# Kernel optimization log

Hardware: AMD Instinct MI355X
Metric: run time of the kernel (lower is better)

## Reference

```python
import jax, jax.numpy as jnp
import numpy as np

N = 50000
IN_CH = 128
OUT_CH = 64
HEADS = 4
NEG_SLOPE = 0.2


def _gatv2(x, src, dst, W_l, W_r, att):
    """GATv2Conv, concat=False, no bias/residual/dropout.
    x: [N, in]; src/dst: [E]; W_l/W_r: [in, H*C]; att: [H, C].
    Returns [N, C] (mean over heads)."""
    n = x.shape[0]
    xl = (x @ W_l).reshape(n, HEADS, OUT_CH)
    xr = (x @ W_r).reshape(n, HEADS, OUT_CH)
    # per-edge message: x_j (source, lin_l) + x_i (target, lin_r)
    m = jax.nn.leaky_relu(xl[src] + xr[dst], negative_slope=NEG_SLOPE)  # [E,H,C]
    e = jnp.einsum('ehc,hc->eh', m, att)  # [E,H]
    # segment softmax over incoming edges of each dst node
    emax = jax.ops.segment_max(e, dst, num_segments=n)  # [N,H] (-inf for empty)
    ex = jnp.exp(e - emax[dst])
    denom = jax.ops.segment_sum(ex, dst, num_segments=n)  # [N,H]
    alpha = ex / denom[dst]
    out = jax.ops.segment_sum(alpha[:, :, None] * xl[src], dst, num_segments=n)  # [N,H,C]
    return out.mean(axis=1)


def setup_inputs() -> dict:
    key = jax.random.key(0)
    ks = jax.random.split(key, 9)
    E = 800000
    s = 1.0 / np.sqrt(IN_CH)
    return {
        'x': jax.random.normal(ks[0], (N, IN_CH), dtype=jnp.float32),
        'edge_index1': jax.random.randint(ks[1], (2, E), 0, N, dtype=jnp.int64),
        'edge_index2': jax.random.randint(ks[2], (2, E), 0, N, dtype=jnp.int64),
        'W_l': jax.random.normal(ks[3], (IN_CH, HEADS * OUT_CH), dtype=jnp.float32) * s,  # shared lin_l
        'W_r0': jax.random.normal(ks[4], (IN_CH, HEADS * OUT_CH), dtype=jnp.float32) * s,
        'W_r1': jax.random.normal(ks[5], (IN_CH, HEADS * OUT_CH), dtype=jnp.float32) * s,
        'att0': jax.random.normal(ks[6], (HEADS, OUT_CH), dtype=jnp.float32) * (1.0 / np.sqrt(OUT_CH)),
        'att1': jax.random.normal(ks[7], (HEADS, OUT_CH), dtype=jnp.float32) * (1.0 / np.sqrt(OUT_CH)),
        'theta': jnp.zeros((1,), dtype=jnp.float32),
    }


def reference(x, edge_index1, edge_index2, W_l, W_r0, W_r1, att0, att1, theta):
    n = x.shape[0]
    # hop 0: add self loops
    loop = jnp.arange(n, dtype=edge_index1.dtype)
    src0 = jnp.concatenate([edge_index1[0], loop])
    dst0 = jnp.concatenate([edge_index1[1], loop])
    out = _gatv2(x, src0, dst0, W_l, W_r0, att0)
    # hop 1: no self loops, gated residual sum
    out = out + jax.nn.sigmoid(theta[0]) * _gatv2(x, edge_index2[0], edge_index2[1], W_l, W_r1, att1)
    return out
```

## Files before the change

kernel.cpp:

```cpp
#include <hip/hip_runtime.h>
#include <hip/hip_bf16.h>
#include <math.h>

#define IN_CH   128
#define HC      256
#define OUT_C   64

typedef unsigned short ushort_t;
typedef __attribute__((ext_vector_type(2))) float v2f;
typedef __attribute__((ext_vector_type(4))) float v4f;
typedef __attribute__((ext_vector_type(8))) short bf16x8;

__device__ __forceinline__ ushort_t f2bf_rne(float f) {
    unsigned u = __float_as_uint(f);
    unsigned r = (u + 0x7FFFu + ((u >> 16) & 1u)) >> 16;
    return (ushort_t)r;
}
__device__ __forceinline__ v2f bfpair(unsigned u) {
    v2f r;
    r.x = __uint_as_float(u << 16);
    r.y = __uint_as_float(u & 0xffff0000u);
    return r;
}
__device__ __forceinline__ v2f vmax0(v2f a) {
    v2f r;
    r.x = fmaxf(a.x, 0.f);
    r.y = fmaxf(a.y, 0.f);
    return r;
}

__device__ __forceinline__ float4 ntld4(const float* p) {
    v4f t = __builtin_nontemporal_load((const v4f*)p);
    return make_float4(t.x, t.y, t.z, t.w);
}
__device__ __forceinline__ int ntldi(const int* p) {
    return __builtin_nontemporal_load(p);
}
__device__ __forceinline__ void ntst4(float* p, float4 v) {
    v4f t = {v.x, v.y, v.z, v.w};
    __builtin_nontemporal_store(t, (v4f*)p);
}
__device__ __forceinline__ void ntsti(int* p, int v) {
    __builtin_nontemporal_store(v, p);
}

#define DPP_ROR_ADD(x, N)                                                   \
    (x) += __uint_as_float(__builtin_amdgcn_update_dpp(                     \
        0, __float_as_uint(x), 0x120 + (N), 0xF, 0xF, true))

__device__ __forceinline__ float rowsum16(float x) {
    DPP_ROR_ADD(x, 8);
    DPP_ROR_ADD(x, 4);
    DPP_ROR_ADD(x, 2);
    DPP_ROR_ADD(x, 1);
    return x;
}

__device__ __forceinline__ bf16x8 ldbf(const uint4* p) {
    union { uint4 u; bf16x8 v; } t;
    t.u = *p;
    return t.v;
}

__device__ __forceinline__ void dev_gemm(const float* __restrict__ x,
                                         const float* __restrict__ W,
                                         float* __restrict__ outf,
                                         ushort_t* __restrict__ outh,
                                         int n, int bx) {
    const int tid = threadIdx.x;
    const int c4  = tid & 63;
    const int rg  = __builtin_amdgcn_readfirstlane(tid >> 6);
    const int row0 = bx * 64 + rg * 16;
    const int nm1 = n - 1;
    const float4* Wv = (const float4*)W;
    const float* xr[16];
#pragma unroll
    for (int j = 0; j < 16; ++j) {
        int r = row0 + j;
        xr[j] = x + (size_t)(r > nm1 ? nm1 : r) * IN_CH;
    }
    v2f acc[16][2];
#pragma unroll
    for (int j = 0; j < 16; ++j) {
        acc[j][0] = (v2f){0.f, 0.f};
        acc[j][1] = (v2f){0.f, 0.f};
    }
    for (int k = 0; k < IN_CH; k += 4) {
        const float4 w0 = Wv[(k + 0) * 64 + c4];
        const float4 w1 = Wv[(k + 1) * 64 + c4];
        const float4 w2 = Wv[(k + 2) * 64 + c4];
        const float4 w3 = Wv[(k + 3) * 64 + c4];
        const v2f w0a = {w0.x, w0.y}, w0b = {w0.z, w0.w};
        const v2f w1a = {w1.x, w1.y}, w1b = {w1.z, w1.w};
        const v2f w2a = {w2.x, w2.y}, w2b = {w2.z, w2.w};
        const v2f w3a = {w3.x, w3.y}, w3b = {w3.z, w3.w};
#pragma unroll
        for (int jb = 0; jb < 2; ++jb) {
            float4 xv[8];
#pragma unroll
            for (int j = 0; j < 8; ++j) xv[j] = *(const float4*)(xr[jb * 8 + j] + k);
#pragma unroll
            for (int j = 0; j < 8; ++j) {
                const int a = jb * 8 + j;
                const v2f s0 = {xv[j].x, xv[j].x}, s1 = {xv[j].y, xv[j].y};
                const v2f s2 = {xv[j].z, xv[j].z}, s3 = {xv[j].w, xv[j].w};
                acc[a][0] = s0 * w0a + acc[a][0];
                acc[a][1] = s0 * w0b + acc[a][1];
                acc[a][0] = s1 * w1a + acc[a][0];
                acc[a][1] = s1 * w1b + acc[a][1];
                acc[a][0] = s2 * w2a + acc[a][0];
                acc[a][1] = s2 * w2b + acc[a][1];
                acc[a][0] = s3 * w3a + acc[a][0];
                acc[a][1] = s3 * w3b + acc[a][1];
            }
        }
    }
#pragma unroll
    for (int j = 0; j < 16; ++j) {
        const int row = row0 + j;
        if (row < n) {
            if (outh) {
                ushort4 h;
                h.x = f2bf_rne(acc[j][0].x);
                h.y = f2bf_rne(acc[j][0].y);
                h.z = f2bf_rne(acc[j][1].x);
                h.w = f2bf_rne(acc[j][1].y);
                ((ushort4*)(outh + (size_t)row * HC))[c4] = h;
            } else {
                ntst4(outf + (size_t)row * HC + 4 * c4,
                      make_float4(acc[j][0].x, acc[j][0].y, acc[j][1].x, acc[j][1].y));
            }
        }
    }
}

__device__ __forceinline__ void dev_scatter_rank(const int* __restrict__ src1,
                                                 const int* __restrict__ dst1, int E1,
                                                 const int* __restrict__ src2,
                                                 const int* __restrict__ dst2, int E2,
                                                 int n, const int* __restrict__ offs,
                                                 const int* __restrict__ rank,
                                                 int* __restrict__ csr,
                                                 int bid, int nB) {
    const int Et = E1 + E2;
    for (int i = bid * 256 + threadIdx.x; i < Et; i += nB * 256) {
        if (i < E1) {
            csr[offs[ntldi(dst1 + i)] + ntldi(rank + i)] = ntldi(src1 + i) << 9;
        } else {
            int j = i - E1;
            csr[offs[n + ntldi(dst2 + j)] + ntldi(rank + i)] = ntldi(src2 + j) << 9;
        }
    }
}

__global__ __launch_bounds__(256) void k_prep(const float* __restrict__ x,
                                              const float* __restrict__ Wl,
                                              const float* __restrict__ Wr0,
                                              const float* __restrict__ Wr1,
                                              uint4* __restrict__ xAh,
                                              uint4* __restrict__ xAl,
                                              uint4* __restrict__ WBh,
                                              uint4* __restrict__ WBl,
                                              int n, int GH, int gPX,
                                              const int* __restrict__ dst1, int E1,
                                              const int* __restrict__ dst2, int E2,
                                              int* __restrict__ deg,
                                              int* __restrict__ rank) {
    const int bx = blockIdx.x;
    if (bx < GH) {
        const int Et = E1 + E2;
        for (int i = bx * 256 + threadIdx.x; i < Et; i += GH * 256) {
            if (i < E1) ntsti(rank + i, atomicAdd(&deg[ntldi(dst1 + i)], 1));
            else        ntsti(rank + i, atomicAdd(&deg[n + ntldi(dst2 + i - E1)], 1));
        }
        return;
    }
    const int t = bx - GH;
    float v[8];
    ushort_t h[8], l[8];
    if (t < gPX) {
        const int idx = t * 256 + threadIdx.x;
        const int row = idx >> 4;
        const int ko  = idx & 15;
        float4 v0 = make_float4(0.f, 0.f, 0.f, 0.f), v1 = v0;
        if (row < n) {
            const float4* xp = (const float4*)(x + (size_t)row * IN_CH + ko * 8);
            v0 = xp[0];
            v1 = xp[1];
        }
        v[0] = v0.x; v[1] = v0.y; v[2] = v0.z; v[3] = v0.w;
        v[4] = v1.x; v[5] = v1.y; v[6] = v1.z; v[7] = v1.w;
#pragma unroll
        for (int j = 0; j < 8; ++j) {
            h[j] = f2bf_rne(v[j]);
            l[j] = f2bf_rne(v[j] - __uint_as_float((unsigned)h[j] << 16));
        }
        const int di = ((row >> 4) * 4 + (ko >> 2)) * 64 + ((ko & 3) << 4) + (row & 15);
        uint4 ph, pl;
        ph.x = (unsigned)h[0] | ((unsigned)h[1] << 16);
        ph.y = (unsigned)h[2] | ((unsigned)h[3] << 16);
        ph.z = (unsigned)h[4] | ((unsigned)h[5] << 16);
        ph.w = (unsigned)h[6] | ((unsigned)h[7] << 16);
        pl.x = (unsigned)l[0] | ((unsigned)l[1] << 16);
        pl.y = (unsigned)l[2] | ((unsigned)l[3] << 16);
        pl.z = (unsigned)l[4] | ((unsigned)l[5] << 16);
        pl.w = (unsigned)l[6] | ((unsigned)l[7] << 16);
        xAh[di] = ph;
        xAl[di] = pl;
    } else {
        const int idx = (t - gPX) * 256 + threadIdx.x;
        const int lane = idx & 63;
        const int f    = (idx >> 6) & 15;
        const int c    = (idx >> 10) & 3;
        const int w    = idx >> 12;
        if (w >= 3) return;
        const float* Wp = (w == 0) ? Wl : ((w == 1) ? Wr0 : Wr1);
        const int col = f * 16 + (lane & 15);
        const int k0  = c * 32 + (lane >> 4) * 8;
#pragma unroll
        for (int j = 0; j < 8; ++j) {
            v[j] = Wp[(size_t)(k0 + j) * HC + col];
            h[j] = f2bf_rne(v[j]);
            l[j] = f2bf_rne(v[j] - __uint_as_float((unsigned)h[j] << 16));
        }
        uint4 ph, pl;
        ph.x = (unsigned)h[0] | ((unsigned)h[1] << 16);
        ph.y = (unsigned)h[2] | ((unsigned)h[3] << 16);
        ph.z = (unsigned)h[4] | ((unsigned)h[5] << 16);
        ph.w = (unsigned)h[6] | ((unsigned)h[7] << 16);
        pl.x = (unsigned)l[0] | ((unsigned)l[1] << 16);
        pl.y = (unsigned)l[2] | ((unsigned)l[3] << 16);
        pl.z = (unsigned)l[4] | ((unsigned)l[5] << 16);
        pl.w = (unsigned)l[6] | ((unsigned)l[7] << 16);
        WBh[idx] = ph;
        WBl[idx] = pl;
    }
}

__global__ __launch_bounds__(256) void k_gemm3(const uint4* __restrict__ xAh,
                                               const uint4* __restrict__ xAl,
                                               const uint4* __restrict__ WBh,
                                               const uint4* __restrict__ WBl,
                                               ushort_t* __restrict__ xlh,
                                               float* __restrict__ xr0,
                                               float* __restrict__ xr1,
                                               int n, int GS,
                                               const int* __restrict__ src1,
                                               const int* __restrict__ dst1, int E1,
                                               const int* __restrict__ src2,
                                               const int* __restrict__ dst2, int E2,
                                               const int* __restrict__ offs,
                                               const int* __restrict__ rank,
                                               int* __restrict__ csr) {
    const int bx = blockIdx.x;
    if (bx < GS) {
        dev_scatter_rank(src1, dst1, E1, src2, dst2, E2, n, offs, rank, csr, bx, GS);
        return;
    }
    const int t    = bx - GS;
    const int tile = t / 3;
    const int wsel = t - tile * 3;

    const int lane = threadIdx.x & 63;
    const int wave = __builtin_amdgcn_readfirstlane((int)(threadIdx.x >> 6));

    v4f acc[4][4];
#pragma unroll
    for (int g = 0; g < 4; ++g)
#pragma unroll
        for (int f = 0; f < 4; ++f) acc[g][f] = (v4f){0.f, 0.f, 0.f, 0.f};

    const uint4* Bh = WBh + (size_t)wsel * 4096;
    const uint4* Bl = WBl + (size_t)wsel * 4096;
    const int g0 = tile * 4;

    for (int c = 0; c < 4; ++c) {
        bf16x8 ah[4], al[4], bh[4], bl[4];
#pragma unroll
        for (int g = 0; g < 4; ++g) {
            const int ai = ((g0 + g) * 4 + c) * 64 + lane;
            ah[g] = ldbf(xAh + ai);
            al[g] = ldbf(xAl + ai);
        }
#pragma unroll
        for (int f = 0; f < 4; ++f) {
            const int bi = (c * 16 + wave * 4 + f) * 64 + lane;
            bh[f] = ldbf(Bh + bi);
            bl[f] = ldbf(Bl + bi);
        }
#pragma unroll
        for (int g = 0; g < 4; ++g)
#pragma unroll
            for (int f = 0; f < 4; ++f) {
                acc[g][f] = __builtin_amdgcn_mfma_f32_16x16x32_bf16(ah[g], bh[f], acc[g][f], 0, 0, 0);
                acc[g][f] = __builtin_amdgcn_mfma_f32_16x16x32_bf16(ah[g], bl[f], acc[g][f], 0, 0, 0);
                acc[g][f] = __builtin_amdgcn_mfma_f32_16x16x32_bf16(al[g], bh[f], acc[g][f], 0, 0, 0);
            }
    }

    const int colB = wave * 64 + (lane & 15);
    const int rowB = tile * 64 + ((lane >> 4) << 2);
    if (wsel == 0) {
#pragma unroll
        for (int g = 0; g < 4; ++g)
#pragma unroll
            for (int f = 0; f < 4; ++f) {
                const int col = colB + f * 16;
#pragma unroll
                for (int r = 0; r < 4; ++r) {
                    const int row = rowB + g * 16 + r;
                    if (row < n) xlh[(size_t)row * HC + col] = f2bf_rne(acc[g][f][r]);
                }
            }
    } else {
        float* o = (wsel == 1) ? xr0 : xr1;
#pragma unroll
        for (int g = 0; g < 4; ++g)
#pragma unroll
            for (int f = 0; f < 4; ++f) {
                const int col = colB + f * 16;
#pragma unroll
                for (int r = 0; r < 4; ++r) {
                    const int row = rowB + g * 16 + r;
                    if (row < n)
                        __builtin_nontemporal_store(acc[g][f][r], o + (size_t)row * HC + col);
                }
            }
    }
}

__global__ __launch_bounds__(256) void k_aggboth(const ushort_t* __restrict__ xlh,
                                                 const float* __restrict__ xr0,
                                                 const float* __restrict__ xr1,
                                                 const float* __restrict__ att0,
                                                 const float* __restrict__ att1,
                                                 const int* __restrict__ offs,
                                                 const int* __restrict__ deg,
                                                 const int* __restrict__ csr,
                                                 int n, float* __restrict__ out,
                                                 const float* __restrict__ theta) {
    const int lane = threadIdx.x & 63;
    int node_ = blockIdx.x * 4 + (threadIdx.x >> 6);
    if (node_ >= n) return;
    const int node = __builtin_amdgcn_readfirstlane(node_);

    const float4 at0 = ((const float4*)att0)[lane];
    const float4 at1 = ((const float4*)att1)[lane];
    const v2f a2_0a = {0.2f * at0.x, 0.2f * at0.y}, a2_0b = {0.2f * at0.z, 0.2f * at0.w};
    const v2f a8_0a = {0.8f * at0.x, 0.8f * at0.y}, a8_0b = {0.8f * at0.z, 0.8f * at0.w};
    const v2f a2_1a = {0.2f * at1.x, 0.2f * at1.y}, a2_1b = {0.2f * at1.z, 0.2f * at1.w};
    const v2f a8_1a = {0.8f * at1.x, 0.8f * at1.y}, a8_1b = {0.8f * at1.z, 0.8f * at1.w};
    const float4 q0 = ntld4(xr0 + (size_t)node * HC + 4 * lane);
    const float4 q1 = ntld4(xr1 + (size_t)node * HC + 4 * lane);
    const v2f x0a = {q0.x, q0.y}, x0b = {q0.z, q0.w};
    const v2f x1a = {q1.x, q1.y}, x1b = {q1.z, q1.w};

    const int t0 = deg[node];
    const int s0 = offs[node];
    const int t1 = deg[n + node];
    const int s1 = offs[n + node];

    const char* Xc = (const char*)xlh;
    const unsigned laneB = (unsigned)lane * 8u;
    auto gat = [&](int off) -> uint2 {
        return *(const uint2*)(Xc + (unsigned)off + laneB);
    };

    float l0 = 0.f, l1 = 0.f;
    v2f O0a = {0.f, 0.f}, O0b = {0.f, 0.f};
    v2f O1a = {0.f, 0.f}, O1b = {0.f, 0.f};

    auto proc = [&](uint2 w, const v2f& xa, const v2f& xb,
                    const v2f& a8a, const v2f& a8b,
                    const v2f& a2a, const v2f& a2b, float& l, v2f& Oa, v2f& Ob) {
        v2f ca = bfpair(w.x), cb = bfpair(w.y);
        v2f za = ca + xa, zb = cb + xb;
        v2f t = a2a * za + a2b * zb + a8a * vmax0(za) + a8b * vmax0(zb);
        float part = rowsum16(t.x + t.y);
        float p = __expf(fminf(part, 60.f));
        l += p;
        v2f pp = {p, p};
        Oa = pp * ca + Oa;
        Ob = pp * cb + Ob;
    };
    auto proc0 = [&](uint2 w) { proc(w, x0a, x0b, a8_0a, a8_0b, a2_0a, a2_0b, l0, O0a, O0b); };
    auto proc1 = [&](uint2 w) { proc(w, x1a, x1b, a8_1a, a8_1b, a2_1a, a2_1b, l1, O1a, O1b); };

    proc0(gat(node << 9));

    auto ld0 = [&](int i) -> uint2 { return gat(ntldi(csr + s0 + i)); };
    auto ld1 = [&](int i) -> uint2 { return gat(ntldi(csr + s1 + i)); };

    uint2 a0 = ld0(0), a1 = ld0(1), a2 = ld0(2), a3 = ld0(3);
    uint2 b0 = ld1(0), b1 = ld1(1), b2 = ld1(2), b3 = ld1(3);

    const int k = t0 < t1 ? t0 : t1;
    int i = 0;
    for (; i + 2 <= k; i += 2) {
        uint2 c0 = a0, c1 = a1, d0 = b0, d1 = b1;
        a0 = a2; a1 = a3;
        b0 = b2; b1 = b3;
        a2 = ld0(i + 4);
        b2 = ld1(i + 4);
        a3 = ld0(i + 5);
        b3 = ld1(i + 5);
        proc0(c0);
        proc1(d0);
        proc0(c1);
        proc1(d1);
    }
    for (int i0 = i; i0 < t0; ++i0) {
        uint2 c = a0;
        a0 = a1; a1 = a2; a2 = a3;
        a3 = ld0(i0 + 4);
        proc0(c);
    }
    for (int i1 = i; i1 < t1; ++i1) {
        uint2 c = b0;
        b0 = b1; b1 = b2; b2 = b3;
        b3 = ld1(i1 + 4);
        proc1(c);
    }

    const float inv0 = 0.25f / l0;
    const float inv1 = (l1 > 0.f) ? 0.25f / l1 : 0.f;
    const float sg = 1.f / (1.f + __expf(-theta[0]));
    float vx = O0a.x * inv0 + sg * (O1a.x * inv1);
    float vy = O0a.y * inv0 + sg * (O1a.y * inv1);
    float vz = O0b.x * inv0 + sg * (O1b.x * inv1);
    float vw = O0b.y * inv0 + sg * (O1b.y * inv1);
    vx += __shfl_xor(vx, 16); vx += __shfl_xor(vx, 32);
    vy += __shfl_xor(vy, 16); vy += __shfl_xor(vy, 32);
    vz += __shfl_xor(vz, 16); vz += __shfl_xor(vz, 32);
    vw += __shfl_xor(vw, 16); vw += __shfl_xor(vw, 32);

    if (lane < 16) {
        ntst4(out + (size_t)node * OUT_C + 4 * lane, make_float4(vx, vy, vz, vw));
    }
}

__device__ __forceinline__ void dev_agg(const ushort_t* __restrict__ xlh,
                                        const float* __restrict__ xr,
                                        const float* __restrict__ att,
                                        const int* __restrict__ offs,
                                        const int* __restrict__ deg,
                                        const int* __restrict__ csr_src,
                                        int n, float* __restrict__ out,
                                        int selfLoop,
                                        const float* __restrict__ theta,
                                        int accumulate, int bid) {
    const int lane = threadIdx.x & 63;
    const int node = bid * 4 + (threadIdx.x >> 6);
    if (node >= n) return;

    const float4 attv = ((const float4*)att)[lane];
    const v2f a2a = {0.2f * attv.x, 0.2f * attv.y}, a2b = {0.2f * attv.z, 0.2f * attv.w};
    const v2f a8a = {0.8f * attv.x, 0.8f * attv.y}, a8b = {0.8f * attv.z, 0.8f * attv.w};
    const float4 q = ntld4(xr + (size_t)node * HC + 4 * lane);
    const v2f xa = {q.x, q.y}, xb = {q.z, q.w};
    const int start2 = offs[node] - selfLoop;
    const int total  = deg[node] + selfLoop;

    float l = 0.f;
    v2f Oa = {0.f, 0.f}, Ob = {0.f, 0.f};
    const char* Xc = (const char*)xlh;
    const unsigned laneB = (unsigned)lane * 8u;

    auto ld = [&](int i) -> uint2 {
        int off = (selfLoop && i == 0) ? (node << 9) : ntldi(csr_src + start2 + i);
        return *(const uint2*)(Xc + (unsigned)off + laneB);
    };
    auto process = [&](uint2 w) {
        v2f ca = bfpair(w.x), cb = bfpair(w.y);
        v2f za = ca + xa, zb = cb + xb;
        v2f t = a2a * za + a2b * zb + a8a * vmax0(za) + a8b * vmax0(zb);
        float part = rowsum16(t.x + t.y);
        float p = __expf(fminf(part, 60.f));
        l += p;
        v2f pp = {p, p};
        Oa = pp * ca + Oa;
        Ob = pp * cb + Ob;
    };

    if (total > 0) {
        uint2 b0 = ld(0);
        uint2 b1 = ld(1);
        uint2 b2 = ld(2);
        uint2 b3 = ld(3);
        int i = 0;
        for (; i + 4 <= total; i += 4) {
            uint2 c0 = b0, c1 = b1, c2 = b2, c3 = b3;
            b0 = ld(i + 4);
            b1 = ld(i + 5);
            b2 = ld(i + 6);
            b3 = ld(i + 7);
            process(c0);
            process(c1);
            process(c2);
            process(c3);
        }
        const int rem = total - i;
        if (rem > 0) process(b0);
        if (rem > 1) process(b1);
        if (rem > 2) process(b2);
    }

    float inv = (l > 0.f) ? 0.25f / l : 0.f;
    float vx = Oa.x * inv, vy = Oa.y * inv, vz = Ob.x * inv, vw = Ob.y * inv;
    vx += __shfl_xor(vx, 16); vx += __shfl_xor(vx, 32);
    vy += __shfl_xor(vy, 16); vy += __shfl_xor(vy, 32);
    vz += __shfl_xor(vz, 16); vz += __shfl_xor(vz, 32);
    vw += __shfl_xor(vw, 16); vw += __shfl_xor(vw, 32);

    if (lane < 16) {
        float4 r = make_float4(vx, vy, vz, vw);
        float4* op = (float4*)(out + (size_t)node * OUT_C);
        if (accumulate) {
            float sg = 1.f / (1.f + __expf(-theta[0]));
            float4 cur = op[lane];
            r.x = fmaf(sg, r.x, cur.x);
            r.y = fmaf(sg, r.y, cur.y);
            r.z = fmaf(sg, r.z, cur.z);
            r.w = fmaf(sg, r.w, cur.w);
        }
        op[lane] = r;
    }
}

__global__ __launch_bounds__(256) void k_mix1(const float* __restrict__ x,
                                              const float* __restrict__ Wa,
                                              ushort_t* __restrict__ oah,
                                              const float* __restrict__ Wb,
                                              float* __restrict__ ob, int n,
                                              int GH, int gG,
                                              const int* __restrict__ dst1, int E1,
                                              const int* __restrict__ dst2, int E2,
                                              int* __restrict__ deg,
                                              int* __restrict__ rank) {
    const int bx = blockIdx.x;
    if (bx < GH) {
        const int Et = E1 + E2;
        for (int i = bx * 256 + threadIdx.x; i < Et; i += GH * 256) {
            if (i < E1) ntsti(rank + i, atomicAdd(&deg[ntldi(dst1 + i)], 1));
            else        ntsti(rank + i, atomicAdd(&deg[n + ntldi(dst2 + i - E1)], 1));
        }
    } else {
        int t = bx - GH;
        if (t < gG) dev_gemm(x, Wa, nullptr, oah, n, t);
        else        dev_gemm(x, Wb, ob, nullptr, n, t - gG);
    }
}

__global__ __launch_bounds__(256) void k_mix2(const float* __restrict__ x,
                                              const float* __restrict__ Wc,
                                              float* __restrict__ oc, int n,
                                              int GS,
                                              const int* __restrict__ src1,
                                              const int* __restrict__ dst1, int E1,
                                              const int* __restrict__ src2,
                                              const int* __restrict__ dst2, int E2,
                                              const int* __restrict__ offs,
                                              const int* __restrict__ rank,
                                              int* __restrict__ csr) {
    const int bx = blockIdx.x;
    if (bx < GS)
        dev_scatter_rank(src1, dst1, E1, src2, dst2, E2, n, offs, rank, csr, bx, GS);
    else
        dev_gemm(x, Wc, oc, nullptr, n, bx - GS);
}

__global__ __launch_bounds__(256) void k_mix3(const ushort_t* __restrict__ xlh,
                                              const float* __restrict__ xr,
                                              const float* __restrict__ att,
                                              const int* __restrict__ offs,
                                              const int* __restrict__ deg,
                                              const int* __restrict__ csr_src,
                                              int n, float* __restrict__ out,
                                              int selfLoop,
                                              const float* __restrict__ theta,
                                              int accumulate) {
    dev_agg(xlh, xr, att, offs, deg, csr_src, n, out, selfLoop, theta,
            accumulate, blockIdx.x);
}

__global__ void k_zero(int* p, int n, int* q, int qn) {
    int i = blockIdx.x * 256 + threadIdx.x;
    if (i < n) p[i] = 0;
    if (blockIdx.x == 0 && threadIdx.x < (unsigned)qn) q[threadIdx.x] = 0;
}

__global__ __launch_bounds__(1024) void k_scanA(const int* __restrict__ deg, int n,
                                                int* __restrict__ incl,
                                                int* __restrict__ bsum) {
    __shared__ int sm[1024];
    const int t = threadIdx.x;
    const int i = blockIdx.x * 1024 + t;
    sm[t] = (i < n) ? deg[i] : 0;
    for (int off = 1; off < 1024; off <<= 1) {
        __syncthreads();
        int u = (t >= off) ? sm[t - off] : 0;
        __syncthreads();
        sm[t] += u;
    }
    if (i < n) incl[i] = sm[t];
    if (t == 1023) bsum[blockIdx.x] = sm[1023];
}

__global__ __launch_bounds__(1024) void k_scanB(int* __restrict__ bsum, int nb) {
    __shared__ int sm[1024];
    const int t = threadIdx.x;
    sm[t] = (t < nb) ? bsum[t] : 0;
    for (int off = 1; off < 1024; off <<= 1) {
        __syncthreads();
        int u = (t >= off) ? sm[t - off] : 0;
        __syncthreads();
        sm[t] += u;
    }
    if (t < nb) bsum[t] = sm[t];
}

__global__ void k_scanCf(const int* __restrict__ incl, const int* __restrict__ deg,
                         const int* __restrict__ bsum, int nb, int n,
                         int* __restrict__ offs) {
    __shared__ int sb[128];
    const int t = threadIdx.x;
    if (t < 128) sb[t] = (t < nb) ? bsum[t] : 0;
    __syncthreads();
#pragma unroll
    for (int off = 1; off < 128; off <<= 1) {
        int u = (t >= off && t < 128) ? sb[t - off] : 0;
        __syncthreads();
        if (t < 128) sb[t] += u;
        __syncthreads();
    }
    int i = blockIdx.x * 256 + t;
    if (i < n) {
        int b    = i >> 10;
        int base = (b > 0) ? sb[b - 1] : 0;
        offs[i] = base + incl[i] - deg[i];
    }
}

__global__ void k_scanC(const int* __restrict__ incl, const int* __restrict__ deg,
                        const int* __restrict__ bsum, int n,
                        int* __restrict__ offs) {
    int i = blockIdx.x * 256 + threadIdx.x;
    if (i < n) {
        int b    = i >> 10;
        int base = (b > 0) ? bsum[b - 1] : 0;
        offs[i] = base + incl[i] - deg[i];
    }
}

extern "C" void kernel_launch(void* const* d_in, const int* in_sizes, int n_in,
                              void* d_out, int out_size, void* d_ws, size_t ws_size,
                              hipStream_t stream) {
    const float* x     = (const float*)d_in[0];
    const int*   e1    = (const int*)d_in[1];
    const int*   e2    = (const int*)d_in[2];
    const float* Wl    = (const float*)d_in[3];
    const float* Wr0   = (const float*)d_in[4];
    const float* Wr1   = (const float*)d_in[5];
    const float* att0  = (const float*)d_in[6];
    const float* att1  = (const float*)d_in[7];
    const float* theta = (const float*)d_in[8];

    const int n  = in_sizes[0] / IN_CH;
    const int E1 = in_sizes[1] / 2;
    const int E2 = in_sizes[2] / 2;
    float* out = (float*)d_out;

    char* w = (char*)d_ws;
    auto alloc = [&](size_t bytes) -> char* {
        char* p = w;
        w += (bytes + 255) & ~(size_t)255;
        return p;
    };
    auto al = [](size_t b) -> size_t { return (b + 255) & ~(size_t)255; };

    const int gT = (n + 63) / 64;
    const size_t projH = (size_t)n * HC * 2;
    const size_t projF = (size_t)n * HC * 4;
    const size_t eB    = (size_t)(E1 + E2) * 4 + 64;
    const size_t degB  = (size_t)2 * n * 4;
    const size_t xAB   = (size_t)gT * 1024 * 16;
    const size_t WBB   = (size_t)3 * 4 * 16 * 64 * 16;

    const size_t need3 = al(projH) + 2 * al(projF) + 2 * al(eB) + 3 * al(degB) + 4096;
    const size_t needM = need3 + 2 * al(xAB) + 2 * al(WBB);
    const bool mfmaPath = ws_size >= needM;
    const bool threeBuf = ws_size >= need3;

    ushort_t* xlh = (ushort_t*)alloc(projH);
    float* xr0 = (float*)alloc(projF);
    float* xr1 = threeBuf ? (float*)alloc(projF) : xr0;
    int* csr  = (int*)alloc(eB);
    int* rank = (int*)alloc(eB);
    int* deg  = (int*)alloc(degB);
    int* offs = (int*)alloc(degB);
    int* tmp  = (int*)alloc(degB);
    int* bsum = (int*)alloc(4096);

    const int GA    = (n + 3) / 4;
    const int GH    = 2048;
    const int GS    = 2048;
    const int n2    = 2 * n;
    const int gN2   = (n2 + 255) / 256;
    const int nScan = (n2 + 1023) / 1024;

    if (mfmaPath) {
        uint4* xAh = (uint4*)alloc(xAB);
        uint4* xAl = (uint4*)alloc(xAB);
        uint4* WBh = (uint4*)alloc(WBB);
        uint4* WBl = (uint4*)alloc(WBB);
        const int gPX = gT * 4;
        const int gPW = 48;

        k_zero<<<gN2, 256, 0, stream>>>(deg, n2, csr + E1 + E2, 16);
        k_prep<<<GH + gPX + gPW, 256, 0, stream>>>(x, Wl, Wr0, Wr1,
                                                   xAh, xAl, WBh, WBl,
                                                   n, GH, gPX,
                                                   e1 + E1, E1, e2 + E2, E2,
                                                   deg, rank);
        k_scanA<<<nScan, 1024, 0, stream>>>(deg, n2, tmp, bsum);
        if (nScan <= 128) {
            k_scanCf<<<gN2, 256, 0, stream>>>(tmp, deg, bsum, nScan, n2, offs);
        } else {
            k_scanB<<<1, 1024, 0, stream>>>(bsum, nScan);
            k_scanC<<<gN2, 256, 0, stream>>>(tmp, deg, bsum, n2, offs);
        }
        k_gemm3<<<GS + 3 * gT, 256, 0, stream>>>(xAh, xAl, WBh, WBl,
                                                 xlh, xr0, xr1, n, GS,
                                                 e1, e1 + E1, E1, e2, e2 + E2, E2,
                                                 offs, rank, csr);
        k_aggboth<<<GA, 256, 0, stream>>>(xlh, xr0, xr1, att0, att1,
                                          offs, deg, csr, n, out, theta);
        return;
    }

    const int gG = gT;
    k_zero<<<gN2, 256, 0, stream>>>(deg, n2, csr + E1 + E2, 16);
    k_mix1<<<GH + 2 * gG, 256, 0, stream>>>(x, Wl, xlh, Wr0, xr0, n, GH, gG,
                                            e1 + E1, E1, e2 + E2, E2, deg, rank);
    k_scanA<<<nScan, 1024, 0, stream>>>(deg, n2, tmp, bsum);
    if (nScan <= 128) {
        k_scanCf<<<gN2, 256, 0, stream>>>(tmp, deg, bsum, nScan, n2, offs);
    } else {
        k_scanB<<<1, 1024, 0, stream>>>(bsum, nScan);
        k_scanC<<<gN2, 256, 0, stream>>>(tmp, deg, bsum, n2, offs);
    }

    if (threeBuf) {
        k_mix2<<<GS + gG, 256, 0, stream>>>(x, Wr1, xr1, n, GS,
                                            e1, e1 + E1, E1, e2, e2 + E2, E2,
                                            offs, rank, csr);
        k_aggboth<<<GA, 256, 0, stream>>>(xlh, xr0, xr1, att0, att1,
                                          offs, deg, csr, n, out, theta);
    } else {
        k_mix2<<<GS, 256, 0, stream>>>(x, Wr1, xr1, n, GS,
                                       e1, e1 + E1, E1, e2, e2 + E2, E2,
                                       offs, rank, csr);
        k_mix3<<<GA, 256, 0, stream>>>(xlh, xr0, att0, offs, deg, csr, n, out,
                                       1, theta, 0);
        k_mix2<<<gG, 256, 0, stream>>>(x, Wr1, xr0, n, 0,
                                       (const int*)nullptr, (const int*)nullptr, 0,
                                       (const int*)nullptr, (const int*)nullptr, 0,
                                       (const int*)nullptr, (const int*)nullptr,
                                       (int*)nullptr);
        k_mix3<<<GA, 256, 0, stream>>>(xlh, xr0, att1, offs + n, deg + n, csr, n, out,
                                       0, theta, 1);
    }
}
```

Measured before the change: 390.5 us.

## Batch CSR index loads per wavefront with readlane broadcast; split prep kernel

The aggregation loop now loads 64 CSR neighbour indices at once, one per lane, and broadcasts each with readlane. It then issues eight independent row gathers before processing them. This replaces the per-edge scalar index loads and the interleaved two-hop software pipeline, aiming for more memory-level parallelism and fewer dependent index loads. The fused prep kernel is split into separate pack and histogram kernels, and the CSR padding is enlarged to 64 entries so the 64-wide index reads stay in bounds. The two hops are now processed sequentially rather than interleaved, and the kernel split adds a launch.

```diff
diff --git a/kernel.cpp b/kernel.cpp
--- a/kernel.cpp
+++ b/kernel.cpp
@@ -153,7 +153,19 @@
     }
 }
 
-__global__ __launch_bounds__(256) void k_prep(const float* __restrict__ x,
+__global__ __launch_bounds__(256) void k_hist(int n, int GH,
+                                              const int* __restrict__ dst1, int E1,
+                                              const int* __restrict__ dst2, int E2,
+                                              int* __restrict__ deg,
+                                              int* __restrict__ rank) {
+    const int Et = E1 + E2;
+    for (int i = blockIdx.x * 256 + threadIdx.x; i < Et; i += GH * 256) {
+        if (i < E1) ntsti(rank + i, atomicAdd(&deg[ntldi(dst1 + i)], 1));
+        else        ntsti(rank + i, atomicAdd(&deg[n + ntldi(dst2 + i - E1)], 1));
+    }
+}
+
+__global__ __launch_bounds__(256) void k_pack(const float* __restrict__ x,
                                               const float* __restrict__ Wl,
                                               const float* __restrict__ Wr0,
                                               const float* __restrict__ Wr1,
@@ -161,21 +173,8 @@
                                               uint4* __restrict__ xAl,
                                               uint4* __restrict__ WBh,
                                               uint4* __restrict__ WBl,
-                                              int n, int GH, int gPX,
-                                              const int* __restrict__ dst1, int E1,
-                                              const int* __restrict__ dst2, int E2,
-                                              int* __restrict__ deg,
-                                              int* __restrict__ rank) {
-    const int bx = blockIdx.x;
-    if (bx < GH) {
-        const int Et = E1 + E2;
-        for (int i = bx * 256 + threadIdx.x; i < Et; i += GH * 256) {
-            if (i < E1) ntsti(rank + i, atomicAdd(&deg[ntldi(dst1 + i)], 1));
-            else        ntsti(rank + i, atomicAdd(&deg[n + ntldi(dst2 + i - E1)], 1));
-        }
-        return;
-    }
-    const int t = bx - GH;
+                                              int n, int gPX) {
+    const int t = blockIdx.x;
     float v[8];
     ushort_t h[8], l[8];
     if (t < gPX) {
@@ -362,8 +361,9 @@
 
     const char* Xc = (const char*)xlh;
     const unsigned laneB = (unsigned)lane * 8u;
-    auto gat = [&](int off) -> uint2 {
-        return *(const uint2*)(Xc + (unsigned)off + laneB);
+    auto gath = [&](unsigned off) -> uint2 {
+        const char* p = Xc + off;
+        return *(const uint2*)(p + laneB);
     };
 
     float l0 = 0.f, l1 = 0.f;
@@ -386,40 +386,54 @@
     auto proc0 = [&](uint2 w) { proc(w, x0a, x0b, a8_0a, a8_0b, a2_0a, a2_0b, l0, O0a, O0b); };
     auto proc1 = [&](uint2 w) { proc(w, x1a, x1b, a8_1a, a8_1b, a2_1a, a2_1b, l1, O1a, O1b); };
 
-    proc0(gat(node << 9));
-
-    auto ld0 = [&](int i) -> uint2 { return gat(ntldi(csr + s0 + i)); };
-    auto ld1 = [&](int i) -> uint2 { return gat(ntldi(csr + s1 + i)); };
-
-    uint2 a0 = ld0(0), a1 = ld0(1), a2 = ld0(2), a3 = ld0(3);
-    uint2 b0 = ld1(0), b1 = ld1(1), b2 = ld1(2), b3 = ld1(3);
-
-    const int k = t0 < t1 ? t0 : t1;
-    int i = 0;
-    for (; i + 2 <= k; i += 2) {
-        uint2 c0 = a0, c1 = a1, d0 = b0, d1 = b1;
-        a0 = a2; a1 = a3;
-        b0 = b2; b1 = b3;
-        a2 = ld0(i + 4);
-        b2 = ld1(i + 4);
-        a3 = ld0(i + 5);
-        b3 = ld1(i + 5);
-        proc0(c0);
-        proc1(d0);
-        proc0(c1);
-        proc1(d1);
-    }
-    for (int i0 = i; i0 < t0; ++i0) {
-        uint2 c = a0;
-        a0 = a1; a1 = a2; a2 = a3;
-        a3 = ld0(i0 + 4);
-        proc0(c);
-    }
-    for (int i1 = i; i1 < t1; ++i1) {
-        uint2 c = b0;
-        b0 = b1; b1 = b2; b2 = b3;
-        b3 = ld1(i1 + 4);
-        proc1(c);
+    proc0(gath((unsigned)node << 9));
+
+    for (int base = 0; base < t0; base += 64) {
+        const unsigned vc = (unsigned)csr[s0 + base + lane];
+        const int m = (t0 - base < 64) ? (t0 - base) : 64;
+        int j = 0;
+        for (; j + 8 <= m; j += 8) {
+            uint2 g0 = gath((unsigned)__builtin_amdgcn_readlane(vc, j + 0));
+            uint2 g1 = gath((unsigned)__builtin_amdgcn_readlane(vc, j + 1));
+            uint2 g2 = gath((unsigned)__builtin_amdgcn_readlane(vc, j + 2));
+            uint2 g3 = gath((unsigned)__builtin_amdgcn_readlane(vc, j + 3));
+            uint2 g4 = gath((unsigned)__builtin_amdgcn_readlane(vc, j + 4));
+            uint2 g5 = gath((unsigned)__builtin_amdgcn_readlane(vc, j + 5));
+            uint2 g6 = gath((unsigned)__builtin_amdgcn_readlane(vc, j + 6));
+            uint2 g7 = gath((unsigned)__builtin_amdgcn_readlane(vc, j + 7));
+            proc0(g0); proc0(g1); proc0(g2); proc0(g3);
+            proc0(g4); proc0(g5); proc0(g6); proc0(g7);
+        }
+        for (; j + 2 <= m; j += 2) {
+            uint2 g0 = gath((unsigned)__builtin_amdgcn_readlane(vc, j + 0));
+            uint2 g1 = gath((unsigned)__builtin_amdgcn_readlane(vc, j + 1));
+            proc0(g0); proc0(g1);
+        }
+        if (j < m) proc0(gath((unsigned)__builtin_amdgcn_readlane(vc, j)));
+    }
+
+    for (int base = 0; base < t1; base += 64) {
+        const unsigned vc = (unsigned)csr[s1 + base + lane];
+        const int m = (t1 - base < 64) ? (t1 - base) : 64;
+        int j = 0;
+        for (; j + 8 <= m; j += 8) {
+            uint2 g0 = gath((unsigned)__builtin_amdgcn_readlane(vc, j + 0));
+            uint2 g1 = gath((unsigned)__builtin_amdgcn_readlane(vc, j + 1));
+            uint2 g2 = gath((unsigned)__builtin_amdgcn_readlane(vc, j + 2));
+            uint2 g3 = gath((unsigned)__builtin_amdgcn_readlane(vc, j + 3));
+            uint2 g4 = gath((unsigned)__builtin_amdgcn_readlane(vc, j + 4));
+            uint2 g5 = gath((unsigned)__builtin_amdgcn_readlane(vc, j + 5));
+            uint2 g6 = gath((unsigned)__builtin_amdgcn_readlane(vc, j + 6));
+            uint2 g7 = gath((unsigned)__builtin_amdgcn_readlane(vc, j + 7));
+            proc1(g0); proc1(g1); proc1(g2); proc1(g3);
+            proc1(g4); proc1(g5); proc1(g6); proc1(g7);
+        }
+        for (; j + 2 <= m; j += 2) {
+            uint2 g0 = gath((unsigned)__builtin_amdgcn_readlane(vc, j + 0));
+            uint2 g1 = gath((unsigned)__builtin_amdgcn_readlane(vc, j + 1));
+            proc1(g0); proc1(g1);
+        }
+        if (j < m) proc1(gath((unsigned)__builtin_amdgcn_readlane(vc, j)));
     }
 
     const float inv0 = 0.25f / l0;
@@ -681,7 +695,7 @@
     const int gT = (n + 63) / 64;
     const size_t projH = (size_t)n * HC * 2;
     const size_t projF = (size_t)n * HC * 4;
-    const size_t eB    = (size_t)(E1 + E2) * 4 + 64;
+    const size_t eB    = (size_t)(E1 + E2) * 4 + 256;
     const size_t degB  = (size_t)2 * n * 4;
     const size_t xAB   = (size_t)gT * 1024 * 16;
     const size_t WBB   = (size_t)3 * 4 * 16 * 64 * 16;
@@ -716,12 +730,10 @@
         const int gPX = gT * 4;
         const int gPW = 48;
 
-        k_zero<<<gN2, 256, 0, stream>>>(deg, n2, csr + E1 + E2, 16);
-        k_prep<<<GH + gPX + gPW, 256, 0, stream>>>(x, Wl, Wr0, Wr1,
-                                                   xAh, xAl, WBh, WBl,
-                                                   n, GH, gPX,
-                                                   e1 + E1, E1, e2 + E2, E2,
-                                                   deg, rank);
+        k_zero<<<gN2, 256, 0, stream>>>(deg, n2, csr + E1 + E2, 64);
+        k_pack<<<gPX + gPW, 256, 0, stream>>>(x, Wl, Wr0, Wr1,
+                                              xAh, xAl, WBh, WBl, n, gPX);
+        k_hist<<<GH, 256, 0, stream>>>(n, GH, e1 + E1, E1, e2 + E2, E2, deg, rank);
         k_scanA<<<nScan, 1024, 0, stream>>>(deg, n2, tmp, bsum);
         if (nScan <= 128) {
             k_scanCf<<<gN2, 256, 0, stream>>>(tmp, deg, bsum, nScan, n2, offs);
@@ -739,7 +751,7 @@
     }
 
     const int gG = gT;
-    k_zero<<<gN2, 256, 0, stream>>>(deg, n2, csr + E1 + E2, 16);
+    k_zero<<<gN2, 256, 0, stream>>>(deg, n2, csr + E1 + E2, 64);
     k_mix1<<<GH + 2 * gG, 256, 0, stream>>>(x, Wl, xlh, Wr0, xr0, n, GH, gG,
                                             e1 + E1, E1, e2 + E2, E2, deg, rank);
     k_scanA<<<nScan, 1024, 0, stream>>>(deg, n2, tmp, bsum);
```

Result: faster. 373.3 us (-4.4%).
